# Kernel optimization log

Measured on AMD Instinct MI355X. Metric: run time of the kernel, lower is better.

## Reference

```python
import jax, jax.numpy as jnp
import numpy as np

N = 50000      # total nodes (cells + row/col/caption nodes across the batch of tables)
E = 500000     # graph edges (row/col cliques, extra edges)
P = 131072     # candidate edge pairs for the edge head
D_LM = 768     # bert-base hidden size
D_MF = 64      # max_freq_emb_size
H = 4          # num_heads per GAT layer
D = 128        # hidden_layer_size per head
DIN = D_LM + D_MF  # 832
DOUT = H * D       # 512


def setup_inputs() -> dict:
    key = jax.random.key(0)
    ks = jax.random.split(key, 32)
    r = lambda k, sh, s=1.0: jax.random.normal(k, sh, jnp.float32) * s
    inp = {}
    inp['cell_h'] = r(ks[0], (N, D_LM))
    inp['pos_emb'] = r(ks[1], (4, D_LM), 0.02)
    inp['mf_emb'] = r(ks[2], (6, D_MF), 0.02)
    # GAT layer 1 (in 832 -> 4 heads x 128), no residual
    inp['W1'] = r(ks[3], (DIN, DOUT), DIN ** -0.5)
    inp['al1'] = r(ks[4], (H, D), D ** -0.5)
    inp['ar1'] = r(ks[5], (H, D), D ** -0.5)
    inp['b1'] = jnp.zeros((DOUT,), jnp.float32)
    # GAT layer 2 (512 -> 4 heads x 128), identity residual
    inp['W2'] = r(ks[6], (DOUT, DOUT), DOUT ** -0.5)
    inp['al2'] = r(ks[7], (H, D), D ** -0.5)
    inp['ar2'] = r(ks[8], (H, D), D ** -0.5)
    inp['b2'] = jnp.zeros((DOUT,), jnp.float32)
    # comp_and_gid head: Linear(512,256)+BN+ReLU+Linear(256,4)
    inp['Wg1'] = r(ks[9], (DOUT, 256), DOUT ** -0.5)
    inp['bg1'] = jnp.zeros((256,), jnp.float32)
    inp['g_gamma'] = jnp.ones((256,), jnp.float32)
    inp['g_beta'] = jnp.zeros((256,), jnp.float32)
    inp['g_mean'] = jnp.zeros((256,), jnp.float32)
    inp['g_var'] = jnp.ones((256,), jnp.float32)
    inp['Wg2'] = r(ks[10], (256, 4), 256 ** -0.5)
    inp['bg2'] = jnp.zeros((4,), jnp.float32)
    # edge head: Linear(1024,256)+BN+ReLU+Linear(256,1)
    inp['We1'] = r(ks[11], (2 * DOUT, 256), (2 * DOUT) ** -0.5)
    inp['be1'] = jnp.zeros((256,), jnp.float32)
    inp['e_gamma'] = jnp.ones((256,), jnp.float32)
    inp['e_beta'] = jnp.zeros((256,), jnp.float32)
    inp['e_mean'] = jnp.zeros((256,), jnp.float32)
    inp['e_var'] = jnp.ones((256,), jnp.float32)
    inp['We2'] = r(ks[12], (256, 1), 256 ** -0.5)
    inp['be2'] = jnp.zeros((1,), jnp.float32)
    # graph structure / index features (constants)
    inp['src'] = jax.random.randint(ks[13], (E,), 0, N, jnp.int32)
    inp['dst'] = jax.random.randint(ks[14], (E,), 0, N, jnp.int32)
    inp['row_pos'] = jax.random.randint(ks[15], (N,), 0, 4, jnp.int32)
    inp['col_pos'] = jax.random.randint(ks[16], (N,), 0, 4, jnp.int32)
    inp['row_mf'] = jax.random.randint(ks[17], (N,), 0, 6, jnp.int32)
    inp['col_mf'] = jax.random.randint(ks[18], (N,), 0, 6, jnp.int32)
    inp['pairs'] = jax.random.randint(ks[19], (P, 2), 0, N, jnp.int32)
    return inp


def _gat(h, W, al, ar, b, src, dst, residual):
    """DGL-style GATConv: LeakyReLU(a_l.Wh_src + a_r.Wh_dst), edge-softmax over dst."""
    n = h.shape[0]
    feat = (h @ W).reshape(n, H, D)                     # [N,H,D]
    el = jnp.sum(feat * al, axis=-1)                    # [N,H]
    er = jnp.sum(feat * ar, axis=-1)                    # [N,H]
    e = jax.nn.leaky_relu(el[src] + er[dst], 0.2)       # [E,H]
    emax = jax.ops.segment_max(e, dst, num_segments=n)  # per-dst max (stability)
    ee = jnp.exp(e - emax[dst])
    denom = jax.ops.segment_sum(ee, dst, num_segments=n)
    alpha = ee / denom[dst]                             # [E,H]
    out = jax.ops.segment_sum(feat[src] * alpha[:, :, None], dst, num_segments=n)  # [N,H,D]
    if residual:
        out = out + h.reshape(n, H, D)                  # identity residual (in==H*D)
    return (out + b.reshape(H, D)).reshape(n, H * D)


def _bn(x, gamma, beta, mean, var):
    return (x - mean) * jax.lax.rsqrt(var + 1e-5) * gamma + beta


def reference(cell_h, pos_emb, mf_emb, W1, al1, ar1, b1, W2, al2, ar2, b2,
              Wg1, bg1, g_gamma, g_beta, g_mean, g_var, Wg2, bg2,
              We1, be1, e_gamma, e_beta, e_mean, e_var, We2, be2,
              src, dst, row_pos, col_pos, row_mf, col_mf, pairs):
    # embedding fusion: LM cell embeddings + row/col positional embeddings
    h = cell_h + pos_emb[row_pos] + pos_emb[col_pos]                    # [N,768]
    mf = mf_emb[jnp.minimum(row_mf, 5)] + mf_emb[jnp.minimum(col_mf, 5)]  # [N,64]
    h = jnp.concatenate([h, mf], axis=-1)                               # [N,832]
    # two multi-head GATConv layers (dropout inactive at eval)
    h = _gat(h, W1, al1, ar1, b1, src, dst, residual=False)             # [N,512]
    h = _gat(h, W2, al2, ar2, b2, src, dst, residual=True)              # [N,512]
    # comp_and_gid head
    gid_logits = jax.nn.relu(_bn(h @ Wg1 + bg1, g_gamma, g_beta, g_mean, g_var)) @ Wg2 + bg2  # [N,4]
    # edge head over candidate node pairs
    ef = jnp.concatenate([h[pairs[:, 0]], h[pairs[:, 1]]], axis=-1)     # [P,1024]
    edge_logits = jax.nn.relu(_bn(ef @ We1 + be1, e_gamma, e_beta, e_mean, e_var)) @ We2 + be2  # [P,1]
    return gid_logits, edge_logits
```

## Files before the change

kernel.cpp:

```cpp
#include <hip/hip_runtime.h>
#include <math.h>


typedef __attribute__((ext_vector_type(8))) short short8;
typedef __attribute__((ext_vector_type(4))) float f32x4;
typedef unsigned short ushort;

#define GLOAD16(g, l)                                                   \
  __builtin_amdgcn_global_load_lds(                                     \
      (const __attribute__((address_space(1))) unsigned int*)(g),       \
      (__attribute__((address_space(3))) unsigned int*)(l), 16, 0, 0)

__device__ __forceinline__ float b2f(ushort h) {
  union { unsigned u; float f; } v; v.u = ((unsigned)h) << 16; return v.f;
}
__device__ __forceinline__ ushort f2b(float f) {
  union { float f; unsigned u; } v; v.f = f;
  unsigned r = v.u + 0x7fffu + ((v.u >> 16) & 1u);
  return (ushort)(r >> 16);
}
__device__ __forceinline__ void up4(uint2 q, float* o) {
  o[0] = b2f((ushort)(q.x & 0xffffu)); o[1] = b2f((ushort)(q.x >> 16));
  o[2] = b2f((ushort)(q.y & 0xffffu)); o[3] = b2f((ushort)(q.y >> 16));
}
__device__ __forceinline__ void up8(uint4 q, float* o) {
  o[0] = b2f((ushort)(q.x & 0xffffu)); o[1] = b2f((ushort)(q.x >> 16));
  o[2] = b2f((ushort)(q.y & 0xffffu)); o[3] = b2f((ushort)(q.y >> 16));
  o[4] = b2f((ushort)(q.z & 0xffffu)); o[5] = b2f((ushort)(q.z >> 16));
  o[6] = b2f((ushort)(q.w & 0xffffu)); o[7] = b2f((ushort)(q.w >> 16));
}
__device__ __forceinline__ uint4 pk8(const float* o) {
  uint4 q;
  q.x = (unsigned)f2b(o[0]) | ((unsigned)f2b(o[1]) << 16);
  q.y = (unsigned)f2b(o[2]) | ((unsigned)f2b(o[3]) << 16);
  q.z = (unsigned)f2b(o[4]) | ((unsigned)f2b(o[5]) << 16);
  q.w = (unsigned)f2b(o[6]) | ((unsigned)f2b(o[7]) << 16);
  return q;
}
__device__ __forceinline__ float warp_sum(float v) {
#pragma unroll
  for (int o = 32; o > 0; o >>= 1) v += __shfl_xor(v, o);
  return v;
}

__global__ __launch_bounds__(256) void embed_kernel(
    const float* __restrict__ cell_h, const float* __restrict__ pos_emb,
    const float* __restrict__ mf_emb,
    const int* __restrict__ row_pos, const int* __restrict__ col_pos,
    const int* __restrict__ row_mf, const int* __restrict__ col_mf,
    ushort* __restrict__ X0, int N)
{
  const int idx = blockIdx.x * 256 + threadIdx.x;
  const int total = N * 104;
  if (idx >= total) return;
  const int n = idx / 104;
  const int c8 = (idx - n * 104) * 8;
  float o[8];
  if (c8 < 768) {
    const int rp = row_pos[n], cp = col_pos[n];
    const float4* pc = (const float4*)(cell_h + (size_t)n * 768 + c8);
    const float4* pr = (const float4*)(pos_emb + (size_t)rp * 768 + c8);
    const float4* pq = (const float4*)(pos_emb + (size_t)cp * 768 + c8);
    float4 c0 = pc[0], c1 = pc[1], r0 = pr[0], r1 = pr[1], q0 = pq[0], q1 = pq[1];
    o[0] = c0.x + r0.x + q0.x; o[1] = c0.y + r0.y + q0.y;
    o[2] = c0.z + r0.z + q0.z; o[3] = c0.w + r0.w + q0.w;
    o[4] = c1.x + r1.x + q1.x; o[5] = c1.y + r1.y + q1.y;
    o[6] = c1.z + r1.z + q1.z; o[7] = c1.w + r1.w + q1.w;
  } else {
    const int rm = min(row_mf[n], 5), cm = min(col_mf[n], 5);
    const int j0 = c8 - 768;
    const float4* pr = (const float4*)(mf_emb + (size_t)rm * 64 + j0);
    const float4* pq = (const float4*)(mf_emb + (size_t)cm * 64 + j0);
    float4 r0 = pr[0], r1 = pr[1], q0 = pq[0], q1 = pq[1];
    o[0] = r0.x + q0.x; o[1] = r0.y + q0.y; o[2] = r0.z + q0.z; o[3] = r0.w + q0.w;
    o[4] = r1.x + q1.x; o[5] = r1.y + q1.y; o[6] = r1.z + q1.z; o[7] = r1.w + q1.w;
  }
  *(uint4*)(X0 + (size_t)n * 832 + c8) = pk8(o);
}

__device__ __forceinline__ void pack_one(
    const float* __restrict__ W, ushort* __restrict__ Wp,
    int idx, int K, int srcN, int colBase, int nTK)
{
  const int c = idx / K, k = idx - c * K;
  const int n = colBase + c;
  const int tn = n >> 7, tk = k >> 6;
  const int sub = (((n >> 4) & 7) << 1) | ((k >> 5) & 1);
  const int lane = (n & 15) | (((k >> 3) & 3) << 4);
  const int j = k & 7;
  const size_t off = (((size_t)(tn * nTK + tk) << 4) + sub) * 512 + lane * 8 + j;
  Wp[off] = f2b(W[(size_t)k * srcN + c]);
}

#define PREP_C0 (832 * 512)
#define PREP_C1 (PREP_C0 + 512 * 512)
#define PREP_C2 (PREP_C1 + 512 * 256)
#define PREP_C3 (PREP_C2 + 512 * 256)
#define PREP_C4 (PREP_C3 + 512 * 256)
__global__ __launch_bounds__(256) void prep_kernel(
    const float* __restrict__ W1, const float* __restrict__ W2,
    const float* __restrict__ Wg1, const float* __restrict__ We1,
    ushort* __restrict__ W1p, ushort* __restrict__ W2p, ushort* __restrict__ Bh,
    const float* __restrict__ be1, const float* __restrict__ eg,
    const float* __restrict__ eb, const float* __restrict__ em,
    const float* __restrict__ ev, float* __restrict__ sa_ext, float* __restrict__ sbv)
{
  const int idx = blockIdx.x * 256 + threadIdx.x;
  if (idx < PREP_C0) {
    pack_one(W1, W1p, idx, 832, 512, 0, 13);
  } else if (idx < PREP_C1) {
    pack_one(W2, W2p, idx - PREP_C0, 512, 512, 0, 8);
  } else if (idx < PREP_C2) {
    pack_one(Wg1, Bh, idx - PREP_C1, 512, 256, 0, 8);
  } else if (idx < PREP_C3) {
    pack_one(We1, Bh, idx - PREP_C2, 512, 256, 256, 8);
  } else if (idx < PREP_C4) {
    pack_one(We1 + 512 * 256, Bh, idx - PREP_C3, 512, 256, 512, 8);
  } else if (idx < PREP_C4 + 256) {
    const int c = idx - PREP_C4;
    const float sa = eg[c] * rsqrtf(ev[c] + 1e-5f);
    sa_ext[c] = sa;
    sa_ext[c + 256] = sa;
    sbv[c] = eb[c] + (be1[c] - em[c]) * sa;
  }
}

template <int EPI, bool ELR>
__global__ __launch_bounds__(512) void mfma_gemm_kernel(
    const ushort* __restrict__ A, const ushort* __restrict__ Bp,
    ushort* __restrict__ C0, ushort* __restrict__ C1,
    int M, int K, int Ncols, int NT, int mtiles,
    const float* __restrict__ bias, const float* __restrict__ gamma,
    const float* __restrict__ beta, const float* __restrict__ mean,
    const float* __restrict__ var, const float* __restrict__ sa_ext,
    const float* __restrict__ al, const float* __restrict__ ar,
    float* __restrict__ elp, float* __restrict__ erp)
{
  __shared__ ushort LDS[32768];
  __shared__ float redS[768];
  const int tid = threadIdx.x;
  const int lane = tid & 63;
  const int wave = tid >> 6;
  const int wm = wave >> 2, wn = wave & 3;

  const int per = NT << 3;
  const int f = blockIdx.x;
  const int sg = f / per;
  const int rem = f - sg * per;
  const int nb = min(8, mtiles - (sg << 3));
  const int band = rem % nb, colt = rem / nb;
  const int m0 = ((sg << 3) + band) << 7;
  const int n0 = colt << 7;
  const int nTK = K >> 6;

  const int rA = lane & 15;
  const int kA = (lane >> 4) << 3;
  const ushort* Aaddr[2];
#pragma unroll
  for (int q = 0; q < 2; ++q) {
    const int a = (wave << 1) + q;
    int row = m0 + ((a >> 1) << 4) + rA;
    if (row >= M) row = 0;
    Aaddr[q] = A + (size_t)row * K + ((a & 1) << 5) + kA;
  }
  const ushort* Baddr = Bp + (((size_t)colt * nTK) << 13)
                        + ((size_t)(wave << 1) << 9) + (lane << 3);

  f32x4 acc[4][2];
#pragma unroll
  for (int i = 0; i < 4; ++i)
#pragma unroll
    for (int j = 0; j < 2; ++j) acc[i][j] = (f32x4){0.f, 0.f, 0.f, 0.f};

  const int nt = K >> 6;

#pragma unroll
  for (int q = 0; q < 2; ++q)
    GLOAD16(Aaddr[q], LDS + (((wave << 1) + q) << 9));
#pragma unroll
  for (int q = 0; q < 2; ++q)
    GLOAD16(Baddr + (q << 9), LDS + 8192 + (((wave << 1) + q) << 9));
  asm volatile("s_waitcnt vmcnt(0)" ::: "memory");
  __builtin_amdgcn_s_barrier();

  int cur = 0;
  for (int t = 0; t < nt; ++t) {
    const int nxt = cur ^ 1;
    if (t + 1 < nt) {
      const int k0n = (t + 1) << 6;
#pragma unroll
      for (int q = 0; q < 2; ++q)
        GLOAD16(Aaddr[q] + k0n, LDS + (nxt << 14) + (((wave << 1) + q) << 9));
#pragma unroll
      for (int q = 0; q < 2; ++q)
        GLOAD16(Baddr + ((size_t)(t + 1) << 13) + (q << 9),
                LDS + (nxt << 14) + 8192 + (((wave << 1) + q) << 9));
    }
    const ushort* Ab = LDS + (cur << 14);
    const ushort* Bb = Ab + 8192;
#pragma unroll
    for (int ks = 0; ks < 2; ++ks) {
      short8 af[4], bf2[2];
#pragma unroll
      for (int x = 0; x < 4; ++x)
        af[x] = *(const short8*)(Ab + ((((wm << 2) + x) * 2 + ks) << 9) + (lane << 3));
#pragma unroll
      for (int y = 0; y < 2; ++y)
        bf2[y] = *(const short8*)(Bb + ((((wn << 1) + y) * 2 + ks) << 9) + (lane << 3));
#pragma unroll
      for (int mf = 0; mf < 4; ++mf)
#pragma unroll
        for (int nf = 0; nf < 2; ++nf)
          acc[mf][nf] = __builtin_amdgcn_mfma_f32_16x16x32_bf16(
              af[mf], bf2[nf], acc[mf][nf], 0, 0, 0);
    }
    asm volatile("s_waitcnt vmcnt(0)" ::: "memory");
    __builtin_amdgcn_s_barrier();
    cur = nxt;
  }

  __syncthreads();
#pragma unroll
  for (int nf = 0; nf < 2; ++nf) {
    const int cl = (((wn << 1) + nf) << 4) + (lane & 15);
    const int col = n0 + cl;
    float sa = 1.f, sb = 0.f;
    bool dorelu = false;
    if (EPI == 1) {
      if (col < 256) {
        const float rs = rsqrtf(var[col] + 1e-5f);
        sa = rs * gamma[col];
        sb = beta[col] + (bias[col] - mean[col]) * sa;
        dorelu = true;
      } else {
        sa = sa_ext[col - 256];
      }
    }
#pragma unroll
    for (int mf = 0; mf < 4; ++mf) {
      const int rl = (((wm << 2) + mf) << 4) + ((lane >> 4) << 2);
#pragma unroll
      for (int j = 0; j < 4; ++j) {
        float v = acc[mf][nf][j];
        if (EPI == 1) { v = fmaf(v, sa, sb); if (dorelu) v = fmaxf(v, 0.f); }
        LDS[(rl + j) * 132 + cl] = f2b(v);
      }
    }
  }
  __syncthreads();
#pragma unroll
  for (int i = 0; i < 4; ++i) {
    const int g = tid + (i << 9);
    const int r = g >> 4, c8 = g & 15;
    const int row = m0 + r;
    if (row >= M) continue;
    const uint4 v = *(const uint4*)(LDS + r * 132 + (c8 << 3));
    const int col = n0 + (c8 << 3);
    if (EPI == 0) {
      *(uint4*)(C0 + (size_t)row * Ncols + col) = v;
    } else {
      if (col < 256) *(uint4*)(C0 + (size_t)row * 256 + col) = v;
      else           *(uint4*)(C1 + (size_t)row * 512 + (col - 256)) = v;
    }
  }

  if (ELR) {
    const int r = tid & 127;
    const int qq = tid >> 7;
    const float* alh = al + colt * 128 + qq * 32;
    const float* arh = ar + colt * 128 + qq * 32;
    const ushort* rowp = LDS + r * 132 + qq * 32;
    float sl = 0.f, sr = 0.f;
#pragma unroll
    for (int c = 0; c < 32; ++c) {
      const float v = b2f(rowp[c]);
      sl = fmaf(v, alh[c], sl);
      sr = fmaf(v, arh[c], sr);
    }
    if (qq) { redS[((qq - 1) << 7) + r] = sl; redS[384 + ((qq - 1) << 7) + r] = sr; }
    __syncthreads();
    if (!qq) {
      const int row = m0 + r;
      if (row < M) {
        elp[(size_t)row * 4 + colt] = sl + redS[r] + redS[128 + r] + redS[256 + r];
        erp[(size_t)row * 4 + colt] = sr + redS[384 + r] + redS[512 + r] + redS[640 + r];
      }
    }
  }
}

__global__ __launch_bounds__(256) void hist_kernel(
    const int* __restrict__ dst, int* __restrict__ counts, int E)
{
  const int e = blockIdx.x * 256 + threadIdx.x;
  if (e < E) atomicAdd(counts + dst[e], 1);
}

__global__ __launch_bounds__(1024) void scan_kernel(
    const int* __restrict__ counts, int* __restrict__ offsets, int N)
{
  __shared__ int sums[1024];
  const int t = threadIdx.x;
  const int chunk = (N + 1023) >> 10;
  const int beg = t * chunk;
  const int end = min(beg + chunk, N);
  int s = 0;
  for (int i = beg; i < end; ++i) s += counts[i];
  sums[t] = s;
  __syncthreads();
  for (int o = 1; o < 1024; o <<= 1) {
    int u = (t >= o) ? sums[t - o] : 0;
    __syncthreads();
    sums[t] += u;
    __syncthreads();
  }
  int run = sums[t] - s;
  for (int i = beg; i < end; ++i) { offsets[i] = run; run += counts[i]; }
  if (t == 1023) offsets[N] = sums[1023];
}

__global__ __launch_bounds__(256) void scatter_kernel(
    const int* __restrict__ src, const int* __restrict__ dst,
    const int* __restrict__ offsets, int* __restrict__ cursor,
    int* __restrict__ csr_src, int E)
{
  const int e = blockIdx.x * 256 + threadIdx.x;
  if (e >= E) return;
  const int d = dst[e];
  const int pos = offsets[d] + atomicAdd(cursor + d, 1);
  csr_src[pos] = src[e];
}

template <bool RES>
__global__ __launch_bounds__(256) void gat_aggregate_kernel(
    const int* __restrict__ csr_src, const int* __restrict__ offsets,
    const float* __restrict__ el, const float* __restrict__ er,
    const ushort* __restrict__ feat, const float* __restrict__ bias,
    const ushort* __restrict__ resid, ushort* __restrict__ out, int N)
{
  __shared__ float eeS[4][1024];
  __shared__ int sS[4][256];
  const int w = threadIdx.x >> 6;
  const int node = (blockIdx.x * 256 + threadIdx.x) >> 6;
  const int lane = threadIdx.x & 63;
  if (node >= N) return;
  const int beg = offsets[node], end = offsets[node + 1];
  const int deg = end - beg;
  const float4 erd = *(const float4*)(er + (size_t)node * 4);
  float* eew = eeS[w];
  int* sw = sS[w];

  float d0 = 0.f, d1 = 0.f, d2 = 0.f, d3 = 0.f;
  for (int i = lane; i < deg; i += 64) {
    const int s = csr_src[beg + i];
    const float4 l = *(const float4*)(el + (size_t)s * 4);
    float x0 = l.x + erd.x, x1 = l.y + erd.y, x2 = l.z + erd.z, x3 = l.w + erd.w;
    x0 = x0 > 0.f ? x0 : 0.2f * x0;
    x1 = x1 > 0.f ? x1 : 0.2f * x1;
    x2 = x2 > 0.f ? x2 : 0.2f * x2;
    x3 = x3 > 0.f ? x3 : 0.2f * x3;
    const float e0 = __expf(x0), e1 = __expf(x1), e2 = __expf(x2), e3 = __expf(x3);
    if (i < 256) {
      float4 ev = {e0, e1, e2, e3};
      *(float4*)(eew + (i << 2)) = ev;
      sw[i] = s;
    }
    d0 += e0; d1 += e1; d2 += e2; d3 += e3;
  }
  d0 = warp_sum(d0); d1 = warp_sum(d1); d2 = warp_sum(d2); d3 = warp_sum(d3);
  const float r0 = 1.f / d0, r1 = 1.f / d1, r2 = 1.f / d2, r3 = 1.f / d3;
  const int h = lane >> 4;
  const float rh = (lane & 32) ? ((lane & 16) ? r3 : r2) : ((lane & 16) ? r1 : r0);
  const float erh = (lane & 32) ? ((lane & 16) ? erd.w : erd.z)
                                : ((lane & 16) ? erd.y : erd.x);

  float a0[8] = {0.f}, a1[8] = {0.f}, a2[8] = {0.f}, a3[8] = {0.f};
  const int cap = min(deg, 256);
  const int main4 = cap & ~3;
  int i = 0;
  for (; i < main4; i += 4) {
    const int s0 = sw[i], s1 = sw[i + 1], s2 = sw[i + 2], s3 = sw[i + 3];
    const float w0 = eew[((i + 0) << 2) | h] * rh;
    const float w1 = eew[((i + 1) << 2) | h] * rh;
    const float w2 = eew[((i + 2) << 2) | h] * rh;
    const float w3 = eew[((i + 3) << 2) | h] * rh;
    const uint4 q0 = *(const uint4*)(feat + (size_t)s0 * 512 + lane * 8);
    const uint4 q1 = *(const uint4*)(feat + (size_t)s1 * 512 + lane * 8);
    const uint4 q2 = *(const uint4*)(feat + (size_t)s2 * 512 + lane * 8);
    const uint4 q3 = *(const uint4*)(feat + (size_t)s3 * 512 + lane * 8);
    float v[8];
    up8(q0, v);
#pragma unroll
    for (int j = 0; j < 8; ++j) a0[j] = fmaf(v[j], w0, a0[j]);
    up8(q1, v);
#pragma unroll
    for (int j = 0; j < 8; ++j) a1[j] = fmaf(v[j], w1, a1[j]);
    up8(q2, v);
#pragma unroll
    for (int j = 0; j < 8; ++j) a2[j] = fmaf(v[j], w2, a2[j]);
    up8(q3, v);
#pragma unroll
    for (int j = 0; j < 8; ++j) a3[j] = fmaf(v[j], w3, a3[j]);
  }
  for (; i < cap; ++i) {
    const int s = sw[i];
    const float aw = eew[(i << 2) | h] * rh;
    const uint4 q = *(const uint4*)(feat + (size_t)s * 512 + lane * 8);
    float v[8];
    up8(q, v);
#pragma unroll
    for (int j = 0; j < 8; ++j) a0[j] = fmaf(v[j], aw, a0[j]);
  }
  for (; i < deg; ++i) {
    const int s = csr_src[beg + i];
    float x = el[(size_t)s * 4 + h] + erh;
    x = x > 0.f ? x : 0.2f * x;
    const float aw = __expf(x) * rh;
    const uint4 q = *(const uint4*)(feat + (size_t)s * 512 + lane * 8);
    float v[8];
    up8(q, v);
#pragma unroll
    for (int j = 0; j < 8; ++j) a0[j] = fmaf(v[j], aw, a0[j]);
  }
#pragma unroll
  for (int j = 0; j < 8; ++j) a0[j] += (a1[j] + a2[j]) + a3[j];

  const float4 b0 = *(const float4*)(bias + lane * 8);
  const float4 b1 = *(const float4*)(bias + lane * 8 + 4);
  a0[0] += b0.x; a0[1] += b0.y; a0[2] += b0.z; a0[3] += b0.w;
  a0[4] += b1.x; a0[5] += b1.y; a0[6] += b1.z; a0[7] += b1.w;
  if (RES) {
    float q[8];
    up8(*(const uint4*)(resid + (size_t)node * 512 + lane * 8), q);
#pragma unroll
    for (int j = 0; j < 8; ++j) a0[j] += q[j];
  }
  *(uint4*)(out + (size_t)node * 512 + lane * 8) = pk8(a0);
}

__global__ __launch_bounds__(256) void gid2_kernel(
    const ushort* __restrict__ g, const float* __restrict__ Wg2,
    const float* __restrict__ bg2, float* __restrict__ out, int N)
{
  const int wv = (blockIdx.x * 256 + threadIdx.x) >> 6;
  const int lane = threadIdx.x & 63;
  if (wv >= N) return;
  float ga[4];
  up4(*(const uint2*)(g + (size_t)wv * 256 + lane * 4), ga);
  float a0 = 0.f, a1 = 0.f, a2 = 0.f, a3 = 0.f;
  const float* wp = Wg2 + (size_t)lane * 16;
#pragma unroll
  for (int j = 0; j < 4; j++) {
    const float4 w = *(const float4*)(wp + j * 4);
    a0 += ga[j] * w.x; a1 += ga[j] * w.y; a2 += ga[j] * w.z; a3 += ga[j] * w.w;
  }
  a0 = warp_sum(a0); a1 = warp_sum(a1); a2 = warp_sum(a2); a3 = warp_sum(a3);
  if (lane == 0) {
    float4 o = {a0 + bg2[0], a1 + bg2[1], a2 + bg2[2], a3 + bg2[3]};
    *(float4*)(out + (size_t)wv * 4) = o;
  }
}

__global__ __launch_bounds__(256) void pair_combine_kernel(
    const ushort* __restrict__ UV, const int* __restrict__ pairs,
    const float* __restrict__ sb, const float* __restrict__ We2,
    const float* __restrict__ be2, float* __restrict__ out, int P)
{
  const int hw = (blockIdx.x * 256 + threadIdx.x) >> 5;
  const int l = threadIdx.x & 31;
  if (hw >= P) return;
  const int p0 = pairs[2 * hw], p1 = pairs[2 * hw + 1];
  float u[8], v[8];
  up8(*(const uint4*)(UV + (size_t)p0 * 512 + l * 8), u);
  up8(*(const uint4*)(UV + (size_t)p1 * 512 + 256 + l * 8), v);
  const float4 sb0 = *(const float4*)(sb + l * 8);
  const float4 sb1 = *(const float4*)(sb + l * 8 + 4);
  const float4 w0 = *(const float4*)(We2 + l * 8);
  const float4 w1 = *(const float4*)(We2 + l * 8 + 4);
  float s = fmaxf(u[0] + v[0] + sb0.x, 0.f) * w0.x
          + fmaxf(u[1] + v[1] + sb0.y, 0.f) * w0.y
          + fmaxf(u[2] + v[2] + sb0.z, 0.f) * w0.z
          + fmaxf(u[3] + v[3] + sb0.w, 0.f) * w0.w
          + fmaxf(u[4] + v[4] + sb1.x, 0.f) * w1.x
          + fmaxf(u[5] + v[5] + sb1.y, 0.f) * w1.y
          + fmaxf(u[6] + v[6] + sb1.z, 0.f) * w1.z
          + fmaxf(u[7] + v[7] + sb1.w, 0.f) * w1.w;
#pragma unroll
  for (int o = 16; o > 0; o >>= 1) s += __shfl_xor(s, o);
  if (l == 0) out[hw] = s + be2[0];
}

extern "C" void kernel_launch(void* const* d_in, const int* in_sizes, int n_in,
                              void* d_out, int out_size, void* d_ws, size_t ws_size,
                              hipStream_t stream) {
  const float* cell_h  = (const float*)d_in[0];
  const float* pos_emb = (const float*)d_in[1];
  const float* mf_emb  = (const float*)d_in[2];
  const float* W1  = (const float*)d_in[3];
  const float* al1 = (const float*)d_in[4];
  const float* ar1 = (const float*)d_in[5];
  const float* b1  = (const float*)d_in[6];
  const float* W2  = (const float*)d_in[7];
  const float* al2 = (const float*)d_in[8];
  const float* ar2 = (const float*)d_in[9];
  const float* b2  = (const float*)d_in[10];
  const float* Wg1 = (const float*)d_in[11];
  const float* bg1 = (const float*)d_in[12];
  const float* g_gamma = (const float*)d_in[13];
  const float* g_beta  = (const float*)d_in[14];
  const float* g_mean  = (const float*)d_in[15];
  const float* g_var   = (const float*)d_in[16];
  const float* Wg2 = (const float*)d_in[17];
  const float* bg2 = (const float*)d_in[18];
  const float* We1 = (const float*)d_in[19];
  const float* be1 = (const float*)d_in[20];
  const float* e_gamma = (const float*)d_in[21];
  const float* e_beta  = (const float*)d_in[22];
  const float* e_mean  = (const float*)d_in[23];
  const float* e_var   = (const float*)d_in[24];
  const float* We2 = (const float*)d_in[25];
  const float* be2 = (const float*)d_in[26];
  const int* src = (const int*)d_in[27];
  const int* dst = (const int*)d_in[28];
  const int* row_pos = (const int*)d_in[29];
  const int* col_pos = (const int*)d_in[30];
  const int* row_mf  = (const int*)d_in[31];
  const int* col_mf  = (const int*)d_in[32];
  const int* pairs   = (const int*)d_in[33];

  const int N = in_sizes[0] / 768;
  const int E = in_sizes[27];
  const int P = in_sizes[33] / 2;

  ushort* X0    = (ushort*)d_ws;
  ushort* featB = X0 + (size_t)N * 832;
  ushort* h1    = featB + (size_t)N * 512;
  ushort* h2    = h1 + (size_t)N * 512;
  ushort* W1p   = h2 + (size_t)N * 512;
  ushort* W2p   = W1p + 512 * 832;
  ushort* Bh    = W2p + 512 * 512;
  float* sa_ext = (float*)(Bh + 768 * 512);
  float* sbv    = sa_ext + 512;
  float* el     = sbv + 256;
  float* er     = el + (size_t)N * 4;
  int* offsets  = (int*)(er + (size_t)N * 4);
  int* counts   = offsets + (N + 1);
  int* cursor   = counts + N;
  int* csr_src  = cursor + N;
  ushort* g_tmp = X0;
  ushort* UV    = featB;

  const int nodeWaves = (N + 3) / 4;
  const int mtiles = (N + 127) / 128;

  hipMemsetAsync(counts, 0, (size_t)(2 * N) * sizeof(int), stream);
  hist_kernel<<<(E + 255) / 256, 256, 0, stream>>>(dst, counts, E);
  scan_kernel<<<1, 1024, 0, stream>>>(counts, offsets, N);
  scatter_kernel<<<(E + 255) / 256, 256, 0, stream>>>(src, dst, offsets, cursor, csr_src, E);

  prep_kernel<<<(PREP_C4 + 256 + 255) / 256, 256, 0, stream>>>(
      W1, W2, Wg1, We1, W1p, W2p, Bh,
      be1, e_gamma, e_beta, e_mean, e_var, sa_ext, sbv);

  embed_kernel<<<(N * 104 + 255) / 256, 256, 0, stream>>>(
      cell_h, pos_emb, mf_emb, row_pos, col_pos, row_mf, col_mf, X0, N);

  mfma_gemm_kernel<0, true><<<mtiles * 4, 512, 0, stream>>>(
      X0, W1p, featB, nullptr, N, 832, 512, 4, mtiles,
      nullptr, nullptr, nullptr, nullptr, nullptr, nullptr, al1, ar1, el, er);
  gat_aggregate_kernel<false><<<nodeWaves, 256, 0, stream>>>(
      csr_src, offsets, el, er, featB, b1, nullptr, h1, N);

  mfma_gemm_kernel<0, true><<<mtiles * 4, 512, 0, stream>>>(
      h1, W2p, featB, nullptr, N, 512, 512, 4, mtiles,
      nullptr, nullptr, nullptr, nullptr, nullptr, nullptr, al2, ar2, el, er);
  gat_aggregate_kernel<true><<<nodeWaves, 256, 0, stream>>>(
      csr_src, offsets, el, er, featB, b2, h1, h2, N);

  mfma_gemm_kernel<1, false><<<mtiles * 6, 512, 0, stream>>>(
      h2, Bh, g_tmp, UV, N, 512, 0, 6, mtiles,
      bg1, g_gamma, g_beta, g_mean, g_var, sa_ext, nullptr, nullptr, nullptr, nullptr);
  gid2_kernel<<<nodeWaves, 256, 0, stream>>>(g_tmp, Wg2, bg2, (float*)d_out, N);
  pair_combine_kernel<<<(P + 7) / 8, 256, 0, stream>>>(
      UV, pairs, sbv, We2, be2, (float*)d_out + (size_t)N * 4, P);
}
```

Baseline: 589.2 us.

## Enlarge GEMM tile to 256 rows and drop LDS double buffering

The MFMA GEMM now computes a 256x128 output tile per block, with each wave owning a 64x64 sub-tile and 16 accumulators instead of 8. This raises data reuse per LDS load and halves the number of row tiles. Global-to-LDS double buffering is removed in favour of a single-buffered load-sync-compute loop, which cuts LDS footprint. The epilogue writes the tile in two 128-row passes. The trade-offs are exposed load latency, higher register pressure and fewer blocks for the scheduler.

```diff
diff --git a/kernel.cpp b/kernel.cpp
--- a/kernel.cpp
+++ b/kernel.cpp
@@ -136,12 +136,12 @@
     const float* __restrict__ al, const float* __restrict__ ar,
     float* __restrict__ elp, float* __restrict__ erp)
 {
-  __shared__ ushort LDS[32768];
+  __shared__ ushort LDS[24576];
   __shared__ float redS[768];
   const int tid = threadIdx.x;
   const int lane = tid & 63;
   const int wave = tid >> 6;
-  const int wm = wave >> 2, wn = wave & 3;
+  const int wm = wave >> 1, wn = wave & 1;
 
   const int per = NT << 3;
   const int f = blockIdx.x;
@@ -149,16 +149,16 @@
   const int rem = f - sg * per;
   const int nb = min(8, mtiles - (sg << 3));
   const int band = rem % nb, colt = rem / nb;
-  const int m0 = ((sg << 3) + band) << 7;
+  const int m0 = ((sg << 3) + band) << 8;
   const int n0 = colt << 7;
   const int nTK = K >> 6;
 
   const int rA = lane & 15;
   const int kA = (lane >> 4) << 3;
-  const ushort* Aaddr[2];
-#pragma unroll
-  for (int q = 0; q < 2; ++q) {
-    const int a = (wave << 1) + q;
+  const ushort* Aaddr[4];
+#pragma unroll
+  for (int q = 0; q < 4; ++q) {
+    const int a = (wave << 2) + q;
     int row = m0 + ((a >> 1) << 4) + rA;
     if (row >= M) row = 0;
     Aaddr[q] = A + (size_t)row * K + ((a & 1) << 5) + kA;
@@ -166,124 +166,114 @@
   const ushort* Baddr = Bp + (((size_t)colt * nTK) << 13)
                         + ((size_t)(wave << 1) << 9) + (lane << 3);
 
-  f32x4 acc[4][2];
+  f32x4 acc[4][4];
 #pragma unroll
   for (int i = 0; i < 4; ++i)
 #pragma unroll
-    for (int j = 0; j < 2; ++j) acc[i][j] = (f32x4){0.f, 0.f, 0.f, 0.f};
+    for (int j = 0; j < 4; ++j) acc[i][j] = (f32x4){0.f, 0.f, 0.f, 0.f};
 
   const int nt = K >> 6;
-
-#pragma unroll
-  for (int q = 0; q < 2; ++q)
-    GLOAD16(Aaddr[q], LDS + (((wave << 1) + q) << 9));
-#pragma unroll
-  for (int q = 0; q < 2; ++q)
-    GLOAD16(Baddr + (q << 9), LDS + 8192 + (((wave << 1) + q) << 9));
-  asm volatile("s_waitcnt vmcnt(0)" ::: "memory");
-  __builtin_amdgcn_s_barrier();
-
-  int cur = 0;
   for (int t = 0; t < nt; ++t) {
-    const int nxt = cur ^ 1;
-    if (t + 1 < nt) {
-      const int k0n = (t + 1) << 6;
-#pragma unroll
-      for (int q = 0; q < 2; ++q)
-        GLOAD16(Aaddr[q] + k0n, LDS + (nxt << 14) + (((wave << 1) + q) << 9));
-#pragma unroll
-      for (int q = 0; q < 2; ++q)
-        GLOAD16(Baddr + ((size_t)(t + 1) << 13) + (q << 9),
-                LDS + (nxt << 14) + 8192 + (((wave << 1) + q) << 9));
+    const int k0 = t << 6;
+#pragma unroll
+    for (int q = 0; q < 4; ++q)
+      GLOAD16(Aaddr[q] + k0, LDS + (((wave << 2) + q) << 9));
+#pragma unroll
+    for (int q = 0; q < 2; ++q)
+      GLOAD16(Baddr + ((size_t)t << 13) + (q << 9),
+              LDS + 16384 + (((wave << 1) + q) << 9));
+    __syncthreads();
+#pragma unroll
+    for (int ks = 0; ks < 2; ++ks) {
+      short8 af[4], bf4[4];
+#pragma unroll
+      for (int x = 0; x < 4; ++x)
+        af[x] = *(const short8*)(LDS + ((((wm << 2) + x) * 2 + ks) << 9) + (lane << 3));
+#pragma unroll
+      for (int y = 0; y < 4; ++y)
+        bf4[y] = *(const short8*)(LDS + 16384 + ((((wn << 2) + y) * 2 + ks) << 9) + (lane << 3));
+#pragma unroll
+      for (int mf = 0; mf < 4; ++mf)
+#pragma unroll
+        for (int nf = 0; nf < 4; ++nf)
+          acc[mf][nf] = __builtin_amdgcn_mfma_f32_16x16x32_bf16(
+              af[mf], bf4[nf], acc[mf][nf], 0, 0, 0);
     }
-    const ushort* Ab = LDS + (cur << 14);
-    const ushort* Bb = Ab + 8192;
-#pragma unroll
-    for (int ks = 0; ks < 2; ++ks) {
-      short8 af[4], bf2[2];
-#pragma unroll
-      for (int x = 0; x < 4; ++x)
-        af[x] = *(const short8*)(Ab + ((((wm << 2) + x) * 2 + ks) << 9) + (lane << 3));
-#pragma unroll
-      for (int y = 0; y < 2; ++y)
-        bf2[y] = *(const short8*)(Bb + ((((wn << 1) + y) * 2 + ks) << 9) + (lane << 3));
-#pragma unroll
-      for (int mf = 0; mf < 4; ++mf)
-#pragma unroll
-        for (int nf = 0; nf < 2; ++nf)
-          acc[mf][nf] = __builtin_amdgcn_mfma_f32_16x16x32_bf16(
-              af[mf], bf2[nf], acc[mf][nf], 0, 0, 0);
-    }
-    asm volatile("s_waitcnt vmcnt(0)" ::: "memory");
-    __builtin_amdgcn_s_barrier();
-    cur = nxt;
-  }
-
-  __syncthreads();
-#pragma unroll
-  for (int nf = 0; nf < 2; ++nf) {
-    const int cl = (((wn << 1) + nf) << 4) + (lane & 15);
-    const int col = n0 + cl;
-    float sa = 1.f, sb = 0.f;
-    bool dorelu = false;
-    if (EPI == 1) {
-      if (col < 256) {
-        const float rs = rsqrtf(var[col] + 1e-5f);
-        sa = rs * gamma[col];
-        sb = beta[col] + (bias[col] - mean[col]) * sa;
-        dorelu = true;
-      } else {
-        sa = sa_ext[col - 256];
+    __syncthreads();
+  }
+
+#pragma unroll
+  for (int p = 0; p < 2; ++p) {
+    __syncthreads();
+    if ((wm >> 1) == p) {
+#pragma unroll
+      for (int nf = 0; nf < 4; ++nf) {
+        const int cl = (((wn << 2) + nf) << 4) + (lane & 15);
+        const int col = n0 + cl;
+        float sa = 1.f, sb = 0.f;
+        bool dorelu = false;
+        if (EPI == 1) {
+          if (col < 256) {
+            const float rs = rsqrtf(var[col] + 1e-5f);
+            sa = rs * gamma[col];
+            sb = beta[col] + (bias[col] - mean[col]) * sa;
+            dorelu = true;
+          } else {
+            sa = sa_ext[col - 256];
+          }
+        }
+#pragma unroll
+        for (int mf = 0; mf < 4; ++mf) {
+          const int rl = ((((wm & 1) << 2) + mf) << 4) + ((lane >> 4) << 2);
+#pragma unroll
+          for (int j = 0; j < 4; ++j) {
+            float v = acc[mf][nf][j];
+            if (EPI == 1) { v = fmaf(v, sa, sb); if (dorelu) v = fmaxf(v, 0.f); }
+            LDS[(rl + j) * 132 + cl] = f2b(v);
+          }
+        }
       }
     }
-#pragma unroll
-    for (int mf = 0; mf < 4; ++mf) {
-      const int rl = (((wm << 2) + mf) << 4) + ((lane >> 4) << 2);
-#pragma unroll
-      for (int j = 0; j < 4; ++j) {
-        float v = acc[mf][nf][j];
-        if (EPI == 1) { v = fmaf(v, sa, sb); if (dorelu) v = fmaxf(v, 0.f); }
-        LDS[(rl + j) * 132 + cl] = f2b(v);
+    __syncthreads();
+    const int rbase = m0 + (p << 7);
+#pragma unroll
+    for (int i = 0; i < 4; ++i) {
+      const int g = tid + (i << 9);
+      const int r = g >> 4, c8 = g & 15;
+      const int row = rbase + r;
+      if (row < M) {
+        const uint4 v = *(const uint4*)(LDS + r * 132 + (c8 << 3));
+        const int col = n0 + (c8 << 3);
+        if (EPI == 0) {
+          *(uint4*)(C0 + (size_t)row * Ncols + col) = v;
+        } else if (col < 256) {
+          *(uint4*)(C0 + (size_t)row * 256 + col) = v;
+        } else {
+          *(uint4*)(C1 + (size_t)row * 512 + (col - 256)) = v;
+        }
       }
     }
-  }
-  __syncthreads();
-#pragma unroll
-  for (int i = 0; i < 4; ++i) {
-    const int g = tid + (i << 9);
-    const int r = g >> 4, c8 = g & 15;
-    const int row = m0 + r;
-    if (row >= M) continue;
-    const uint4 v = *(const uint4*)(LDS + r * 132 + (c8 << 3));
-    const int col = n0 + (c8 << 3);
-    if (EPI == 0) {
-      *(uint4*)(C0 + (size_t)row * Ncols + col) = v;
-    } else {
-      if (col < 256) *(uint4*)(C0 + (size_t)row * 256 + col) = v;
-      else           *(uint4*)(C1 + (size_t)row * 512 + (col - 256)) = v;
-    }
-  }
-
-  if (ELR) {
-    const int r = tid & 127;
-    const int qq = tid >> 7;
-    const float* alh = al + colt * 128 + qq * 32;
-    const float* arh = ar + colt * 128 + qq * 32;
-    const ushort* rowp = LDS + r * 132 + qq * 32;
-    float sl = 0.f, sr = 0.f;
-#pragma unroll
-    for (int c = 0; c < 32; ++c) {
-      const float v = b2f(rowp[c]);
-      sl = fmaf(v, alh[c], sl);
-      sr = fmaf(v, arh[c], sr);
-    }
-    if (qq) { redS[((qq - 1) << 7) + r] = sl; redS[384 + ((qq - 1) << 7) + r] = sr; }
-    __syncthreads();
-    if (!qq) {
-      const int row = m0 + r;
-      if (row < M) {
-        elp[(size_t)row * 4 + colt] = sl + redS[r] + redS[128 + r] + redS[256 + r];
-        erp[(size_t)row * 4 + colt] = sr + redS[384 + r] + redS[512 + r] + redS[640 + r];
+    if (ELR) {
+      const int r = tid & 127;
+      const int qq = tid >> 7;
+      const float* alh = al + colt * 128 + qq * 32;
+      const float* arh = ar + colt * 128 + qq * 32;
+      const ushort* rowp = LDS + r * 132 + qq * 32;
+      float sl = 0.f, sr = 0.f;
+#pragma unroll
+      for (int c = 0; c < 32; ++c) {
+        const float v = b2f(rowp[c]);
+        sl = fmaf(v, alh[c], sl);
+        sr = fmaf(v, arh[c], sr);
+      }
+      if (qq) { redS[((qq - 1) << 7) + r] = sl; redS[384 + ((qq - 1) << 7) + r] = sr; }
+      __syncthreads();
+      if (!qq) {
+        const int row = rbase + r;
+        if (row < M) {
+          elp[(size_t)row * 4 + colt] = sl + redS[r] + redS[128 + r] + redS[256 + r];
+          erp[(size_t)row * 4 + colt] = sr + redS[384 + r] + redS[512 + r] + redS[640 + r];
+        }
       }
     }
   }
@@ -551,7 +541,7 @@
   ushort* UV    = featB;
 
   const int nodeWaves = (N + 3) / 4;
-  const int mtiles = (N + 127) / 128;
+  const int mtiles = (N + 255) / 256;
 
   hipMemsetAsync(counts, 0, (size_t)(2 * N) * sizeof(int), stream);
   hist_kernel<<<(E + 255) / 256, 256, 0, stream>>>(dst, counts, E);
```

Result: no change. 586.6 us, median of 2 (-0.4%).
